# Performance work log

Measured on AMD Instinct MI355X. Metric: run time of the kernel, lower is better.

Reference implementation:

```python
import jax, jax.numpy as jnp
import numpy as np

N_NODES = 100000
N_EDGES = 3200000
N_IN = 128
N_HID = 128
N_OUT = 64
HOP = 10


def setup_inputs() -> dict:
    key = jax.random.key(0)
    ks = jax.random.split(key, 8)
    x = jax.random.normal(ks[0], (N_NODES, N_IN), dtype=jnp.float32)
    edge_row = jax.random.randint(ks[1], (N_EDGES,), 0, N_NODES, dtype=jnp.int32)
    edge_col = jax.random.randint(ks[2], (N_EDGES,), 0, N_NODES, dtype=jnp.int32)
    # normalized-ish edge weights so 10 hops of propagation stay bounded
    edge_val = jax.random.uniform(ks[3], (N_EDGES,), dtype=jnp.float32) / 32.0
    s_ih = 1.0 / np.sqrt(N_IN)
    s_hh = 1.0 / np.sqrt(N_HID)
    W_ih = jax.random.normal(ks[4], (4 * N_HID, N_IN), dtype=jnp.float32) * s_ih
    W_hh = jax.random.normal(ks[5], (4 * N_HID, N_HID), dtype=jnp.float32) * s_hh
    b_ih = jnp.zeros((4 * N_HID,), dtype=jnp.float32)
    b_hh = jnp.zeros((4 * N_HID,), dtype=jnp.float32)
    fc_w = jax.random.normal(ks[6], (N_OUT, N_HID), dtype=jnp.float32) * s_hh
    fc_b = jnp.zeros((N_OUT,), dtype=jnp.float32)
    return dict(x=x, edge_row=edge_row, edge_col=edge_col, edge_val=edge_val,
                W_ih=W_ih, W_hh=W_hh, b_ih=b_ih, b_hh=b_hh, fc_w=fc_w, fc_b=fc_b)


def _lstm_cell(x, h, c, W_ih, W_hh, b_ih, b_hh):
    # torch LSTMCell gate order: input, forget, cell(g), output
    gates = x @ W_ih.T + b_ih + h @ W_hh.T + b_hh  # [N, 4H]
    i, f, g, o = jnp.split(gates, 4, axis=-1)
    i = jax.nn.sigmoid(i)
    f = jax.nn.sigmoid(f)
    g = jnp.tanh(g)
    o = jax.nn.sigmoid(o)
    c_new = f * c + i * g
    h_new = o * jnp.tanh(c_new)
    return h_new, c_new


def _spmm(edge_row, edge_col, edge_val, h, n_nodes):
    # (A @ h)[r] = sum_{edges e with row r} val[e] * h[col[e]]
    msgs = edge_val[:, None] * h[edge_col]  # [E, H] gather
    return jax.ops.segment_sum(msgs, edge_row, num_segments=n_nodes)


def reference(x, edge_row, edge_col, edge_val, W_ih, W_hh, b_ih, b_hh, fc_w, fc_b):
    n = x.shape[0]
    h = jnp.zeros((n, W_hh.shape[1]), dtype=x.dtype)
    c = jnp.zeros_like(h)
    # hop iterations: LSTM gate update then sparse propagation (dropout = eval/identity)
    for _ in range(HOP):
        h, c = _lstm_cell(x, h, c, W_ih, W_hh, b_ih, b_hh)
        h = _spmm(edge_row, edge_col, edge_val, h, n)
    h = jax.nn.relu(h)
    return h @ fc_w.T + fc_b
```

## Files before the change

kernel.cpp:

```cpp
#include <hip/hip_runtime.h>
#include <hip/hip_bf16.h>
#include <math.h>

constexpr int NN  = 100000;
constexpr int EE  = 3200000;
constexpr int HID = 128;
constexpr int NG  = 512;
constexpr int NOUT = 64;
constexpr int HOPS = 10;
constexpr int SCAN_BLK = 1024;
constexpr int NBLK_SCAN = (NN + SCAN_BLK - 1) / SCAN_BLK;
constexpr int NB = (NN + 255) / 256;
constexpr int PA_BATCH = 4096;
constexpr int PA_GRID = (EE + PA_BATCH - 1) / PA_BATCH;

typedef __attribute__((ext_vector_type(8))) short short8;
typedef __attribute__((ext_vector_type(4))) float f32x4;

__device__ __forceinline__ ushort f2bf(float f) {
    uint u = __builtin_bit_cast(uint, f);
    u += 0x7fff + ((u >> 16) & 1);
    return (ushort)(u >> 16);
}
__device__ __forceinline__ float bflo(uint u) { return __builtin_bit_cast(float, u << 16); }
__device__ __forceinline__ float bfhi(uint u) { return __builtin_bit_cast(float, u & 0xffff0000u); }

__device__ __forceinline__ float sigf(float v) { return 1.0f / (1.0f + __expf(-v)); }
__device__ __forceinline__ float tanh_fast(float x) {
    float t = __expf(-2.0f * fabsf(x));
    float r = (1.0f - t) / (1.0f + t);
    return copysignf(r, x);
}

__device__ __forceinline__ short8 load_frag(const ushort* p) {
    return *reinterpret_cast<const short8*>(p);
}
__device__ __forceinline__ f32x4 mfma16(short8 a, short8 b, f32x4 c) {
    return __builtin_amdgcn_mfma_f32_16x16x32_bf16(a, b, c, 0, 0, 0);
}

__global__ __launch_bounds__(256) void convert_bf16_kernel(
    const float* __restrict__ src, ushort* __restrict__ dst, int n4)
{
    int i = blockIdx.x * 256 + threadIdx.x;
    if (i < n4) {
        float4 v = reinterpret_cast<const float4*>(src)[i];
        ushort4 o;
        o.x = f2bf(v.x); o.y = f2bf(v.y); o.z = f2bf(v.z); o.w = f2bf(v.w);
        reinterpret_cast<ushort4*>(dst)[i] = o;
    }
}

__global__ __launch_bounds__(256) void bsum_kernel(
    const float* __restrict__ bih, const float* __restrict__ bhh, float* __restrict__ bsum)
{
    int i = blockIdx.x * 256 + threadIdx.x;
    if (i < NG) bsum[i] = bih[i] + bhh[i];
}

__global__ __launch_bounds__(256) void hist_kernel(const int* __restrict__ erow,
                                                   int* __restrict__ deg)
{
    int e = blockIdx.x * 256 + threadIdx.x;
    atomicAdd(&deg[erow[e]], 1);
}

__global__ __launch_bounds__(SCAN_BLK) void scan1_kernel(const int* __restrict__ deg,
                                                         int* __restrict__ bsums)
{
    __shared__ int tmp[SCAN_BLK];
    int t = threadIdx.x;
    int i = blockIdx.x * SCAN_BLK + t;
    tmp[t] = (i < NN) ? deg[i] : 0;
    __syncthreads();
    for (int off = SCAN_BLK / 2; off > 0; off >>= 1) {
        if (t < off) tmp[t] += tmp[t + off];
        __syncthreads();
    }
    if (t == 0) bsums[blockIdx.x] = tmp[0];
}

__global__ __launch_bounds__(128) void scan2_kernel(int* __restrict__ bsums)
{
    __shared__ int tmp[128];
    int t = threadIdx.x;
    tmp[t] = (t < NBLK_SCAN) ? bsums[t] : 0;
    __syncthreads();
    for (int off = 1; off < 128; off <<= 1) {
        int add = (t >= off) ? tmp[t - off] : 0;
        __syncthreads();
        tmp[t] += add;
        __syncthreads();
    }
    if (t < NBLK_SCAN) bsums[t] = (t == 0) ? 0 : tmp[t - 1];
}

__global__ __launch_bounds__(SCAN_BLK) void scan3_kernel(const int* __restrict__ deg,
                                                         const int* __restrict__ bsums,
                                                         int* __restrict__ rp,
                                                         int* __restrict__ cur)
{
    __shared__ int tmp[SCAN_BLK];
    int t = threadIdx.x;
    int i = blockIdx.x * SCAN_BLK + t;
    int v = (i < NN) ? deg[i] : 0;
    tmp[t] = v;
    __syncthreads();
    for (int off = 1; off < SCAN_BLK; off <<= 1) {
        int add = (t >= off) ? tmp[t - off] : 0;
        __syncthreads();
        tmp[t] += add;
        __syncthreads();
    }
    int incl = tmp[t] + bsums[blockIdx.x];
    if (i < NN) {
        rp[i + 1] = incl;
        cur[i] = incl - v;
    }
    if (i == 0) rp[0] = 0;
}

__global__ __launch_bounds__(512) void binit_kernel(const int* __restrict__ rp,
                                                    int* __restrict__ bcur)
{
    int b = threadIdx.x;
    if (b < NB) bcur[b] = rp[b << 8];
}

__global__ __launch_bounds__(256) void passA_kernel(
    const int* __restrict__ erow, const int* __restrict__ ecol,
    const float* __restrict__ eval, int* __restrict__ bcur,
    int* __restrict__ trow, int2* __restrict__ tcv)
{
    __shared__ int  lhist[512];
    __shared__ int  sa[512];
    __shared__ int  sb[512];
    __shared__ int  gbase[512];
    __shared__ int  srow[PA_BATCH];
    __shared__ int2 scv[PA_BATCH];

    const int t = threadIdx.x;
    const int base = blockIdx.x * PA_BATCH;
    const int nb = min(PA_BATCH, EE - base);

    lhist[t] = 0; lhist[t + 256] = 0;
    __syncthreads();

    int er[16], ec[16], pk[16];
    float ev[16];
#pragma unroll
    for (int k = 0; k < 16; ++k) {
        int idx = k * 256 + t;
        if (idx < nb) {
            int e = base + idx;
            int r = erow[e];
            er[k] = r; ec[k] = ecol[e]; ev[k] = eval[e];
            int b = r >> 8;
            int pos = atomicAdd(&lhist[b], 1);
            pk[k] = b | (pos << 9);
        } else pk[k] = -1;
    }
    __syncthreads();

    sa[t] = lhist[t]; sa[t + 256] = lhist[t + 256];
    __syncthreads();
    int* src = sa; int* dst = sb;
    for (int off = 1; off < 512; off <<= 1) {
        dst[t] = src[t] + ((t >= off) ? src[t - off] : 0);
        int i2 = t + 256;
        dst[i2] = src[i2] + src[i2 - off];
        __syncthreads();
        int* tp = src; src = dst; dst = tp;
    }
    int* incl = src;

    for (int b = t; b < NB; b += 256) {
        int cnt = lhist[b];
        gbase[b] = cnt ? atomicAdd(&bcur[b], cnt) : 0;
    }
    __syncthreads();

#pragma unroll
    for (int k = 0; k < 16; ++k) {
        if (pk[k] >= 0) {
            int b = pk[k] & 511;
            int pos = pk[k] >> 9;
            int lofs = b ? incl[b - 1] : 0;
            int s = lofs + pos;
            srow[s] = er[k];
            scv[s] = int2{ec[k], __builtin_bit_cast(int, ev[k])};
        }
    }
    __syncthreads();

    for (int s = t; s < nb; s += 256) {
        int rr = srow[s];
        int b = rr >> 8;
        int lofs = b ? incl[b - 1] : 0;
        int g = gbase[b] + (s - lofs);
        trow[g] = rr;
        tcv[g] = scv[s];
    }
}

__global__ __launch_bounds__(256) void passB_kernel(
    const int* __restrict__ trow, const int2* __restrict__ tcv,
    int* __restrict__ cur, int2* __restrict__ epack)
{
    int e = blockIdx.x * 256 + threadIdx.x;
    int r = trow[e];
    int2 cv = tcv[e];
    int p = atomicAdd(&cur[r], 1);
    epack[p] = cv;
}

template<bool FIRST>
__global__ __launch_bounds__(256, 2) void cell_kernel(
    const ushort* __restrict__ xb, const ushort* __restrict__ hb,
    const ushort* __restrict__ Wib, const ushort* __restrict__ Whb,
    const float* __restrict__ bsum, float* __restrict__ cperm,
    ushort* __restrict__ hout)
{
    __shared__ __align__(16) ushort lds_h[32 * 136];

    const int t  = threadIdx.x;
    const int l  = t & 63;
    const int w  = t >> 6;
    const int lr = l & 15;
    const int lk = l >> 4;
    const int row0 = blockIdx.x * 32;

    f32x4 acc[8][2];
#pragma unroll
    for (int nI = 0; nI < 8; ++nI) {
        float b = bsum[(4 * nI + w) * 16 + lr];
        acc[nI][0] = f32x4{b, b, b, b};
        acc[nI][1] = f32x4{b, b, b, b};
    }

    short8 ax[2][4];
    short8 ah[2][4];
#pragma unroll
    for (int rf = 0; rf < 2; ++rf) {
        const size_t arow = (size_t)(row0 + rf * 16 + lr) * HID + lk * 8;
#pragma unroll
        for (int ks = 0; ks < 4; ++ks) {
            ax[rf][ks] = load_frag(xb + arow + ks * 32);
            if (!FIRST) ah[rf][ks] = load_frag(hb + arow + ks * 32);
        }
    }

#pragma unroll
    for (int nI = 0; nI < 8; ++nI) {
        const int n = 4 * nI + w;
        const ushort* wip = Wib + (size_t)(n * 16 + lr) * HID + lk * 8;
        const ushort* whp = Whb + (size_t)(n * 16 + lr) * HID + lk * 8;
        short8 bi[4], bh[4];
#pragma unroll
        for (int ks = 0; ks < 4; ++ks) {
            bi[ks] = load_frag(wip + ks * 32);
            if (!FIRST) bh[ks] = load_frag(whp + ks * 32);
        }
#pragma unroll
        for (int rf = 0; rf < 2; ++rf) {
#pragma unroll
            for (int ks = 0; ks < 4; ++ks) {
                acc[nI][rf] = mfma16(ax[rf][ks], bi[ks], acc[nI][rf]);
                if (!FIRST) acc[nI][rf] = mfma16(ah[rf][ks], bh[ks], acc[nI][rf]);
            }
        }
    }

#pragma unroll
    for (int nj = 0; nj < 2; ++nj) {
        const int col = (w + 4 * nj) * 16 + lr;
#pragma unroll
        for (int rf = 0; rf < 2; ++rf) {
            f32x4 iv = acc[nj][rf];
            f32x4 fv = acc[nj + 2][rf];
            f32x4 gv = acc[nj + 4][rf];
            f32x4 ov = acc[nj + 6][rf];
            const size_t cidx = ((((size_t)blockIdx.x * 4 + w) * 2 + nj) * 2 + rf) * 64 + l;
            f32x4 cold;
            if (FIRST) cold = f32x4{0.f, 0.f, 0.f, 0.f};
            else       cold = reinterpret_cast<const f32x4*>(cperm)[cidx];
            f32x4 cn, hn;
#pragma unroll
            for (int jj = 0; jj < 4; ++jj) {
                float c2 = sigf(fv[jj]) * cold[jj] + sigf(iv[jj]) * tanh_fast(gv[jj]);
                cn[jj] = c2;
                hn[jj] = sigf(ov[jj]) * tanh_fast(c2);
            }
            reinterpret_cast<f32x4*>(cperm)[cidx] = cn;
            const int rbase = rf * 16 + lk * 4;
#pragma unroll
            for (int jj = 0; jj < 4; ++jj)
                lds_h[(rbase + jj) * 136 + col] = f2bf(hn[jj]);
        }
    }
    __syncthreads();
    {
        const ushort* lsrc = &lds_h[(t >> 3) * 136 + (t & 7) * 16];
        short8 v0 = *reinterpret_cast<const short8*>(lsrc);
        short8 v1 = *reinterpret_cast<const short8*>(lsrc + 8);
        ushort* gdst = hout + (size_t)row0 * HID + t * 16;
        *reinterpret_cast<short8*>(gdst) = v0;
        *reinterpret_cast<short8*>(gdst + 8) = v1;
    }
}

__global__ __launch_bounds__(256) void spmm_kernel(
    const int* __restrict__ rp, const int2* __restrict__ epack,
    const ushort* __restrict__ hin, ushort* __restrict__ hout)
{
    int r = blockIdx.x * 4 + (threadIdx.x >> 6);
    if (r >= NN) return;
    int l = threadIdx.x & 63;
    int beg = rp[r], end = rp[r + 1];
    const unsigned long long* eq = reinterpret_cast<const unsigned long long*>(epack);

    float s0a = 0.f, s1a = 0.f, s0b = 0.f, s1b = 0.f;
    float s0c = 0.f, s1c = 0.f, s0d = 0.f, s1d = 0.f;
    int e = beg;
    for (; e + 4 <= end; e += 4) {
        unsigned long long u0 = __builtin_nontemporal_load(eq + e);
        unsigned long long u1 = __builtin_nontemporal_load(eq + e + 1);
        unsigned long long u2 = __builtin_nontemporal_load(eq + e + 2);
        unsigned long long u3 = __builtin_nontemporal_load(eq + e + 3);
        int c0 = (int)(uint)u0, c1 = (int)(uint)u1, c2 = (int)(uint)u2, c3 = (int)(uint)u3;
        float v0 = __builtin_bit_cast(float, (uint)(u0 >> 32));
        float v1 = __builtin_bit_cast(float, (uint)(u1 >> 32));
        float v2 = __builtin_bit_cast(float, (uint)(u2 >> 32));
        float v3 = __builtin_bit_cast(float, (uint)(u3 >> 32));
        uint g0 = *reinterpret_cast<const uint*>(hin + (size_t)c0 * HID + l * 2);
        uint g1 = *reinterpret_cast<const uint*>(hin + (size_t)c1 * HID + l * 2);
        uint g2 = *reinterpret_cast<const uint*>(hin + (size_t)c2 * HID + l * 2);
        uint g3 = *reinterpret_cast<const uint*>(hin + (size_t)c3 * HID + l * 2);
        s0a += v0 * bflo(g0); s1a += v0 * bfhi(g0);
        s0b += v1 * bflo(g1); s1b += v1 * bfhi(g1);
        s0c += v2 * bflo(g2); s1c += v2 * bfhi(g2);
        s0d += v3 * bflo(g3); s1d += v3 * bfhi(g3);
    }
    for (; e < end; ++e) {
        unsigned long long u0 = __builtin_nontemporal_load(eq + e);
        int c0 = (int)(uint)u0;
        float v0 = __builtin_bit_cast(float, (uint)(u0 >> 32));
        uint g0 = *reinterpret_cast<const uint*>(hin + (size_t)c0 * HID + l * 2);
        s0a += v0 * bflo(g0); s1a += v0 * bfhi(g0);
    }
    float s0 = (s0a + s0b) + (s0c + s0d);
    float s1 = (s1a + s1b) + (s1c + s1d);
    uint o = ((uint)f2bf(s1) << 16) | (uint)f2bf(s0);
    *reinterpret_cast<uint*>(hout + (size_t)r * HID + l * 2) = o;
}

__global__ __launch_bounds__(256) void final_mfma_kernel(
    const ushort* __restrict__ hb, const ushort* __restrict__ fcwb,
    const float* __restrict__ fcb, float* __restrict__ out)
{
    const int t = threadIdx.x;
    const int l = t & 63;
    const int w = t >> 6;
    const int lr = l & 15;
    const int lk = l >> 4;
    const int row0 = blockIdx.x * 64 + w * 16;

    f32x4 acc[4];
#pragma unroll
    for (int n = 0; n < 4; ++n) {
        float b = fcb[n * 16 + lr];
        acc[n] = f32x4{b, b, b, b};
    }

    const short8 z8 = {0, 0, 0, 0, 0, 0, 0, 0};
    const int arow = row0 + lr;
    const bool aok = arow < NN;
    short8 a[4];
#pragma unroll
    for (int ks = 0; ks < 4; ++ks) {
        short8 v = aok ? load_frag(hb + (size_t)arow * HID + ks * 32 + lk * 8) : z8;
#pragma unroll
        for (int i = 0; i < 8; ++i) {
            ushort u = (ushort)v[i];
            if (u & 0x8000) v[i] = 0;
        }
        a[ks] = v;
    }

#pragma unroll
    for (int n = 0; n < 4; ++n) {
        const ushort* wp = fcwb + (size_t)(n * 16 + lr) * HID + lk * 8;
#pragma unroll
        for (int ks = 0; ks < 4; ++ks)
            acc[n] = mfma16(a[ks], load_frag(wp + ks * 32), acc[n]);
    }

#pragma unroll
    for (int n = 0; n < 4; ++n) {
#pragma unroll
        for (int j = 0; j < 4; ++j) {
            int row = row0 + lk * 4 + j;
            if (row < NN) out[(size_t)row * NOUT + n * 16 + lr] = acc[n][j];
        }
    }
}

extern "C" void kernel_launch(void* const* d_in, const int* in_sizes, int n_in,
                              void* d_out, int out_size, void* d_ws, size_t ws_size,
                              hipStream_t stream)
{
    const float* x    = (const float*)d_in[0];
    const int*   erow = (const int*)d_in[1];
    const int*   ecol = (const int*)d_in[2];
    const float* eval = (const float*)d_in[3];
    const float* Wih  = (const float*)d_in[4];
    const float* Whh  = (const float*)d_in[5];
    const float* bih  = (const float*)d_in[6];
    const float* bhh  = (const float*)d_in[7];
    const float* fcw  = (const float*)d_in[8];
    const float* fcb  = (const float*)d_in[9];
    float* out = (float*)d_out;

    char* ws = (char*)d_ws;
    size_t off = 0;
    auto alloc = [&](size_t bytes) -> void* {
        void* p = ws + off;
        off = (off + bytes + 255) & ~(size_t)255;
        return p;
    };
    ushort* hb_a  = (ushort*)alloc((size_t)NN * HID * 2);
    ushort* hb_b  = (ushort*)alloc((size_t)NN * HID * 2);
    float*  cperm = (float*)alloc((size_t)NN * HID * 4);
    ushort* xb    = (ushort*)alloc((size_t)NN * HID * 2);
    ushort* Wib   = (ushort*)alloc((size_t)NG * HID * 2);
    ushort* Whb   = (ushort*)alloc((size_t)NG * HID * 2);
    ushort* fcwb  = (ushort*)alloc((size_t)NOUT * HID * 2);
    float*  bsum  = (float*)alloc((size_t)NG * 4);
    int*    rp    = (int*)alloc((size_t)(NN + 1) * 4);
    int*    deg   = (int*)alloc((size_t)NN * 4);
    int*    cur   = (int*)alloc((size_t)NN * 4);
    int*    bsums = (int*)alloc((size_t)NBLK_SCAN * 4);
    int*    bcur  = (int*)alloc((size_t)NB * 4);
    int2*   epack = (int2*)alloc((size_t)EE * 8);
    (void)ws_size;

    int2* tcv  = (int2*)cperm;
    int*  trow = (int*)((char*)cperm + (size_t)EE * 8);

    convert_bf16_kernel<<<(NN * HID / 4 + 255) / 256, 256, 0, stream>>>(x, xb, NN * HID / 4);
    convert_bf16_kernel<<<(NG * HID / 4 + 255) / 256, 256, 0, stream>>>(Wih, Wib, NG * HID / 4);
    convert_bf16_kernel<<<(NG * HID / 4 + 255) / 256, 256, 0, stream>>>(Whh, Whb, NG * HID / 4);
    convert_bf16_kernel<<<(NOUT * HID / 4 + 255) / 256, 256, 0, stream>>>(fcw, fcwb, NOUT * HID / 4);
    bsum_kernel<<<2, 256, 0, stream>>>(bih, bhh, bsum);

    hipMemsetAsync(deg, 0, (size_t)NN * 4, stream);
    hist_kernel<<<EE / 256, 256, 0, stream>>>(erow, deg);
    scan1_kernel<<<NBLK_SCAN, SCAN_BLK, 0, stream>>>(deg, bsums);
    scan2_kernel<<<1, 128, 0, stream>>>(bsums);
    scan3_kernel<<<NBLK_SCAN, SCAN_BLK, 0, stream>>>(deg, bsums, rp, cur);
    binit_kernel<<<1, 512, 0, stream>>>(rp, bcur);
    passA_kernel<<<PA_GRID, 256, 0, stream>>>(erow, ecol, eval, bcur, trow, tcv);
    passB_kernel<<<EE / 256, 256, 0, stream>>>(trow, tcv, cur, epack);

    const int CELL_GRID = NN / 32;

    cell_kernel<true><<<CELL_GRID, 256, 0, stream>>>(xb, hb_b, Wib, Whb, bsum, cperm, hb_a);
    spmm_kernel<<<(NN + 3) / 4, 256, 0, stream>>>(rp, epack, hb_a, hb_b);
    for (int hop = 1; hop < HOPS; ++hop) {
        cell_kernel<false><<<CELL_GRID, 256, 0, stream>>>(xb, hb_b, Wib, Whb, bsum, cperm, hb_a);
        spmm_kernel<<<(NN + 3) / 4, 256, 0, stream>>>(rp, epack, hb_a, hb_b);
    }

    final_mfma_kernel<<<(NN + 63) / 64, 256, 0, stream>>>(hb_b, fcwb, fcb, out);
}
```

Before: 2.945 ms.

## Split SpMM feature columns across blocks and stage cell GEMM to cut registers

The SpMM kernel now runs two blocks per group of four rows. Each block covers one 64-column half of the feature vector, and within a wave the two 32-lane halves process alternating edges, combined by a shuffle at the end. This gives more blocks and more independent gathers in flight, and each hin gather touches a 128-byte half-row. In exchange every edge record is read twice across the two column halves. The cell kernel splits the x and h GEMM phases with a sched_barrier so the x and h fragments are not live at the same time, and raises launch bounds to 3 blocks per SM to increase occupancy.

```diff
diff --git a/kernel.cpp b/kernel.cpp
--- a/kernel.cpp
+++ b/kernel.cpp
@@ -16,6 +16,7 @@
 
 typedef __attribute__((ext_vector_type(8))) short short8;
 typedef __attribute__((ext_vector_type(4))) float f32x4;
+typedef unsigned long long ull;
 
 __device__ __forceinline__ ushort f2bf(float f) {
     uint u = __builtin_bit_cast(uint, f);
@@ -215,7 +216,7 @@
 }
 
 template<bool FIRST>
-__global__ __launch_bounds__(256, 2) void cell_kernel(
+__global__ __launch_bounds__(256, 3) void cell_kernel(
     const ushort* __restrict__ xb, const ushort* __restrict__ hb,
     const ushort* __restrict__ Wib, const ushort* __restrict__ Whb,
     const float* __restrict__ bsum, float* __restrict__ cperm,
@@ -238,36 +239,51 @@
         acc[nI][1] = f32x4{b, b, b, b};
     }
 
-    short8 ax[2][4];
-    short8 ah[2][4];
-#pragma unroll
-    for (int rf = 0; rf < 2; ++rf) {
-        const size_t arow = (size_t)(row0 + rf * 16 + lr) * HID + lk * 8;
-#pragma unroll
-        for (int ks = 0; ks < 4; ++ks) {
-            ax[rf][ks] = load_frag(xb + arow + ks * 32);
-            if (!FIRST) ah[rf][ks] = load_frag(hb + arow + ks * 32);
-        }
-    }
-
-#pragma unroll
-    for (int nI = 0; nI < 8; ++nI) {
-        const int n = 4 * nI + w;
-        const ushort* wip = Wib + (size_t)(n * 16 + lr) * HID + lk * 8;
-        const ushort* whp = Whb + (size_t)(n * 16 + lr) * HID + lk * 8;
-        short8 bi[4], bh[4];
-#pragma unroll
-        for (int ks = 0; ks < 4; ++ks) {
-            bi[ks] = load_frag(wip + ks * 32);
-            if (!FIRST) bh[ks] = load_frag(whp + ks * 32);
-        }
+    {
+        short8 ax[2][4];
 #pragma unroll
         for (int rf = 0; rf < 2; ++rf) {
-#pragma unroll
-            for (int ks = 0; ks < 4; ++ks) {
-                acc[nI][rf] = mfma16(ax[rf][ks], bi[ks], acc[nI][rf]);
-                if (!FIRST) acc[nI][rf] = mfma16(ah[rf][ks], bh[ks], acc[nI][rf]);
-            }
+            const size_t arow = (size_t)(row0 + rf * 16 + lr) * HID + lk * 8;
+#pragma unroll
+            for (int ks = 0; ks < 4; ++ks)
+                ax[rf][ks] = load_frag(xb + arow + ks * 32);
+        }
+#pragma unroll
+        for (int nI = 0; nI < 8; ++nI) {
+            const int n = 4 * nI + w;
+            const ushort* wip = Wib + (size_t)(n * 16 + lr) * HID + lk * 8;
+            short8 bi[4];
+#pragma unroll
+            for (int ks = 0; ks < 4; ++ks) bi[ks] = load_frag(wip + ks * 32);
+#pragma unroll
+            for (int rf = 0; rf < 2; ++rf)
+#pragma unroll
+                for (int ks = 0; ks < 4; ++ks)
+                    acc[nI][rf] = mfma16(ax[rf][ks], bi[ks], acc[nI][rf]);
+        }
+    }
+    __builtin_amdgcn_sched_barrier(0);
+    if (!FIRST) {
+        short8 ah[2][4];
+#pragma unroll
+        for (int rf = 0; rf < 2; ++rf) {
+            const size_t arow = (size_t)(row0 + rf * 16 + lr) * HID + lk * 8;
+#pragma unroll
+            for (int ks = 0; ks < 4; ++ks)
+                ah[rf][ks] = load_frag(hb + arow + ks * 32);
+        }
+#pragma unroll
+        for (int nI = 0; nI < 8; ++nI) {
+            const int n = 4 * nI + w;
+            const ushort* whp = Whb + (size_t)(n * 16 + lr) * HID + lk * 8;
+            short8 bh[4];
+#pragma unroll
+            for (int ks = 0; ks < 4; ++ks) bh[ks] = load_frag(whp + ks * 32);
+#pragma unroll
+            for (int rf = 0; rf < 2; ++rf)
+#pragma unroll
+                for (int ks = 0; ks < 4; ++ks)
+                    acc[nI][rf] = mfma16(ah[rf][ks], bh[ks], acc[nI][rf]);
         }
     }
 
@@ -313,45 +329,56 @@
     const int* __restrict__ rp, const int2* __restrict__ epack,
     const ushort* __restrict__ hin, ushort* __restrict__ hout)
 {
-    int r = blockIdx.x * 4 + (threadIdx.x >> 6);
+    const int task = blockIdx.x;
+    const int half = task & 1;
+    const int w = threadIdx.x >> 6;
+    const int r = (task >> 1) * 4 + w;
     if (r >= NN) return;
-    int l = threadIdx.x & 63;
-    int beg = rp[r], end = rp[r + 1];
-    const unsigned long long* eq = reinterpret_cast<const unsigned long long*>(epack);
+    const int l = threadIdx.x & 63;
+    const int g = l >> 5;
+    const int fp = l & 31;
+    const ushort* hbase = hin + half * 64 + fp * 2;
+    const int beg = rp[r], end = rp[r + 1];
+    const ull* eq = reinterpret_cast<const ull*>(epack);
 
     float s0a = 0.f, s1a = 0.f, s0b = 0.f, s1b = 0.f;
     float s0c = 0.f, s1c = 0.f, s0d = 0.f, s1d = 0.f;
     int e = beg;
-    for (; e + 4 <= end; e += 4) {
-        unsigned long long u0 = __builtin_nontemporal_load(eq + e);
-        unsigned long long u1 = __builtin_nontemporal_load(eq + e + 1);
-        unsigned long long u2 = __builtin_nontemporal_load(eq + e + 2);
-        unsigned long long u3 = __builtin_nontemporal_load(eq + e + 3);
-        int c0 = (int)(uint)u0, c1 = (int)(uint)u1, c2 = (int)(uint)u2, c3 = (int)(uint)u3;
+    for (; e + 8 <= end; e += 8) {
+        ull u0 = __builtin_nontemporal_load(eq + e + 0 + g);
+        ull u1 = __builtin_nontemporal_load(eq + e + 2 + g);
+        ull u2 = __builtin_nontemporal_load(eq + e + 4 + g);
+        ull u3 = __builtin_nontemporal_load(eq + e + 6 + g);
         float v0 = __builtin_bit_cast(float, (uint)(u0 >> 32));
         float v1 = __builtin_bit_cast(float, (uint)(u1 >> 32));
         float v2 = __builtin_bit_cast(float, (uint)(u2 >> 32));
         float v3 = __builtin_bit_cast(float, (uint)(u3 >> 32));
-        uint g0 = *reinterpret_cast<const uint*>(hin + (size_t)c0 * HID + l * 2);
-        uint g1 = *reinterpret_cast<const uint*>(hin + (size_t)c1 * HID + l * 2);
-        uint g2 = *reinterpret_cast<const uint*>(hin + (size_t)c2 * HID + l * 2);
-        uint g3 = *reinterpret_cast<const uint*>(hin + (size_t)c3 * HID + l * 2);
+        uint g0 = *reinterpret_cast<const uint*>(hbase + (size_t)(uint)u0 * HID);
+        uint g1 = *reinterpret_cast<const uint*>(hbase + (size_t)(uint)u1 * HID);
+        uint g2 = *reinterpret_cast<const uint*>(hbase + (size_t)(uint)u2 * HID);
+        uint g3 = *reinterpret_cast<const uint*>(hbase + (size_t)(uint)u3 * HID);
         s0a += v0 * bflo(g0); s1a += v0 * bfhi(g0);
         s0b += v1 * bflo(g1); s1b += v1 * bfhi(g1);
         s0c += v2 * bflo(g2); s1c += v2 * bfhi(g2);
         s0d += v3 * bflo(g3); s1d += v3 * bfhi(g3);
     }
-    for (; e < end; ++e) {
-        unsigned long long u0 = __builtin_nontemporal_load(eq + e);
-        int c0 = (int)(uint)u0;
-        float v0 = __builtin_bit_cast(float, (uint)(u0 >> 32));
-        uint g0 = *reinterpret_cast<const uint*>(hin + (size_t)c0 * HID + l * 2);
-        s0a += v0 * bflo(g0); s1a += v0 * bfhi(g0);
+    for (; e < end; e += 2) {
+        int idx = e + g;
+        if (idx < end) {
+            ull u0 = __builtin_nontemporal_load(eq + idx);
+            float v0 = __builtin_bit_cast(float, (uint)(u0 >> 32));
+            uint g0 = *reinterpret_cast<const uint*>(hbase + (size_t)(uint)u0 * HID);
+            s0a += v0 * bflo(g0); s1a += v0 * bfhi(g0);
+        }
     }
     float s0 = (s0a + s0b) + (s0c + s0d);
     float s1 = (s1a + s1b) + (s1c + s1d);
-    uint o = ((uint)f2bf(s1) << 16) | (uint)f2bf(s0);
-    *reinterpret_cast<uint*>(hout + (size_t)r * HID + l * 2) = o;
+    s0 += __shfl_xor(s0, 32);
+    s1 += __shfl_xor(s1, 32);
+    if (l < 32) {
+        uint o = ((uint)f2bf(s1) << 16) | (uint)f2bf(s0);
+        *reinterpret_cast<uint*>(hout + (size_t)r * HID + half * 64 + fp * 2) = o;
+    }
 }
 
 __global__ __launch_bounds__(256) void final_mfma_kernel(
@@ -463,12 +490,13 @@
     passB_kernel<<<EE / 256, 256, 0, stream>>>(trow, tcv, cur, epack);
 
     const int CELL_GRID = NN / 32;
+    const int SPMM_GRID = 2 * (NN / 4);
 
     cell_kernel<true><<<CELL_GRID, 256, 0, stream>>>(xb, hb_b, Wib, Whb, bsum, cperm, hb_a);
-    spmm_kernel<<<(NN + 3) / 4, 256, 0, stream>>>(rp, epack, hb_a, hb_b);
+    spmm_kernel<<<SPMM_GRID, 256, 0, stream>>>(rp, epack, hb_a, hb_b);
     for (int hop = 1; hop < HOPS; ++hop) {
         cell_kernel<false><<<CELL_GRID, 256, 0, stream>>>(xb, hb_b, Wib, Whb, bsum, cperm, hb_a);
-        spmm_kernel<<<(NN + 3) / 4, 256, 0, stream>>>(rp, epack, hb_a, hb_b);
+        spmm_kernel<<<SPMM_GRID, 256, 0, stream>>>(rp, epack, hb_a, hb_b);
     }
 
     final_mfma_kernel<<<(NN + 63) / 64, 256, 0, stream>>>(hb_b, fcwb, fcb, out);
```

Result: slower. 3.506 ms (+19.1%).
